# Performance work log

Measured on AMD Instinct MI355X. Metric: run time of the kernel, lower is better.

The kernel has to match this reference:

```python
import jax, jax.numpy as jnp
import numpy as np

WORKSPACE_RADIUS = 1.0
WORKSPACE_HEIGHT = 1.0


def setup_inputs() -> dict:
    key = jax.random.key(0)
    k1, k2 = jax.random.split(key)
    # (B, N, 6): xyz + normals, already padded to common length N
    pointclouds = jax.random.normal(k1, (32, 131072, 6), dtype=jnp.float32)
    # (B, 4, 4): homogeneous task transforms
    task_transform = jax.random.normal(k2, (32, 4, 4), dtype=jnp.float32)
    return {"pointclouds": pointclouds, "task_transform": task_transform}


def reference(pointclouds, task_transform):
    # Split xyz points and normals
    pts = pointclouds[..., :3]          # (B, N, 3)
    nrm = pointclouds[..., 3:]          # (B, N, 3)

    rot = task_transform[:, :3, :3]     # (B, 3, 3)
    trans = task_transform[:, :3, 3]    # (B, 3)

    # points @ rotation + translation (matches torch.matmul(points, rotation))
    p = jnp.einsum('bnd,bde->bne', pts, rot) + trans[:, None, :]

    # padded rows have all-zero normals
    non_padded = jnp.sum(nrm, axis=-1) != 0

    sq_dist = p[..., 0] ** 2 + p[..., 1] ** 2
    in_range = (sq_dist < WORKSPACE_RADIUS ** 2) & (p[..., 2] < WORKSPACE_HEIGHT)
    valid = in_range & non_padded      # (B, N)

    # Filter-and-repad: compact valid points to the front (stable = order
    # preserving, as in the torch boolean-index version), zero the tail.
    order = jnp.argsort(~valid, axis=1, stable=True)                 # (B, N)
    gathered = jnp.take_along_axis(pointclouds, order[..., None], axis=1)
    mask_sorted = jnp.take_along_axis(valid, order, axis=1)
    return gathered * mask_sorted[..., None].astype(pointclouds.dtype)
```

## Files before the change

### kernel.cpp

```cpp
#include <hip/hip_runtime.h>
#include <cstdint>

namespace {

constexpr int kB   = 32;
constexpr int kN   = 131072;
constexpr int kC   = 6;
constexpr int TPB  = 256;
constexpr int ROWS_PER_BLK = 512;
constexpr int BPB  = kN / ROWS_PER_BLK;
constexpr int NBLK = kB * BPB;
constexpr int WAVES = TPB / 64;
constexpr int F4_PER_BLK = ROWS_PER_BLK * kC / 4;

__device__ __forceinline__ int waveSum(int v) {
#pragma unroll
    for (int off = 32; off; off >>= 1) v += __shfl_xor(v, off, 64);
    return v;
}


__global__ __launch_bounds__(TPB) void k_count_stage(const float* __restrict__ pc,
                                                     const float* __restrict__ tt,
                                                     float* __restrict__ staged,
                                                     int* __restrict__ blkCnt) {
    const int blk  = blockIdx.x;
    const int b    = blk >> 8;
    const int tid  = threadIdx.x;
    const int lane = tid & 63;
    const int wv   = tid >> 6;

    const float* T = tt + b * 16;
    const float T0 = T[0], T1 = T[1], T2 = T[2],  T3  = T[3];
    const float T4 = T[4], T5 = T[5], T6 = T[6],  T7  = T[7];
    const float T8 = T[8], T9 = T[9], T10 = T[10], T11 = T[11];

    const float4* f4 = (const float4*)pc + (size_t)blk * F4_PER_BLK;
    const float4 qa = f4[tid];
    const float4 qb = f4[tid + 256];
    const float4 qc = f4[tid + 512];

    __shared__ float4 sb[F4_PER_BLK];
    sb[tid] = qa; sb[tid + 256] = qb; sb[tid + 512] = qc;
    __syncthreads();

    const float2* s2 = (const float2*)sb;
    const float2 r0a = s2[6 * tid],     r0b = s2[6 * tid + 1], r0c = s2[6 * tid + 2];
    const float2 r1a = s2[6 * tid + 3], r1b = s2[6 * tid + 4], r1c = s2[6 * tid + 5];

    const float ns0 = (r0b.y + r0c.x) + r0c.y;
    const float px0 = r0a.x * T0 + r0a.y * T4 + r0b.x * T8  + T3;
    const float py0 = r0a.x * T1 + r0a.y * T5 + r0b.x * T9  + T7;
    const float pz0 = r0a.x * T2 + r0a.y * T6 + r0b.x * T10 + T11;
    const bool v0 = (px0 * px0 + py0 * py0 < 1.0f) && (pz0 < 1.0f) && (ns0 != 0.0f);

    const float ns1 = (r1b.y + r1c.x) + r1c.y;
    const float px1 = r1a.x * T0 + r1a.y * T4 + r1b.x * T8  + T3;
    const float py1 = r1a.x * T1 + r1a.y * T5 + r1b.x * T9  + T7;
    const float pz1 = r1a.x * T2 + r1a.y * T6 + r1b.x * T10 + T11;
    const bool v1 = (px1 * px1 + py1 * py1 < 1.0f) && (pz1 < 1.0f) && (ns1 != 0.0f);

    const uint64_t m0 = __ballot(v0);
    const uint64_t m1 = __ballot(v1);

    __shared__ uint64_t sm[WAVES * 2];
    if (lane == 0) { sm[wv * 2] = m0; sm[wv * 2 + 1] = m1; }
    __syncthreads();

    if (wv == 0) {
        int v = (lane < 8) ? __popcll(sm[lane]) : 0;
        v = waveSum(v);
        if (lane == 0) blkCnt[blk] = v;
    }

    int wb = 0;
#pragma unroll
    for (int w = 0; w < WAVES - 1; ++w)
        if (w < wv) wb += __popcll(sm[w * 2]) + __popcll(sm[w * 2 + 1]);
    const uint64_t low = (1ull << lane) - 1ull;
    const int beforeE = __popcll(m0 & low) + __popcll(m1 & low);
    const int rk0 = wb + beforeE;
    const int rk1 = rk0 + (v0 ? 1 : 0);

    float2* st = (float2*)(staged + (size_t)blk * (ROWS_PER_BLK * kC));
    if (v0) { float2* o = st + rk0 * 3; o[0] = r0a; o[1] = r0b; o[2] = r0c; }
    if (v1) { float2* o = st + rk1 * 3; o[0] = r1a; o[1] = r1b; o[2] = r1c; }
}

__global__ __launch_bounds__(TPB) void k_emit(const float* __restrict__ staged,
                                              const int* __restrict__ blkCnt,
                                              float* __restrict__ out) {
    const int blk  = blockIdx.x;
    const int b    = blk >> 8;
    const int sub  = blk & (BPB - 1);
    const int tid  = threadIdx.x;
    const int lane = tid & 63;
    const int wv   = tid >> 6;

    __shared__ int sRed[2 * WAVES];

    const int c = blkCnt[b * BPB + tid];
    const int pw = waveSum((tid < sub) ? c : 0);
    const int tw = waveSum(c);
    if (lane == 0) { sRed[wv] = pw; sRed[WAVES + wv] = tw; }
    __syncthreads();
    const int blockBase = (sRed[0] + sRed[1]) + (sRed[2] + sRed[3]);
    const int total     = (sRed[4] + sRed[5]) + (sRed[6] + sRed[7]);
    const int myCnt     = blkCnt[blk];

    const size_t batchF = (size_t)b * kN * kC;

    const float2* src = (const float2*)(staged + (size_t)blk * (ROWS_PER_BLK * kC));
    float2* dst = (float2*)(out + batchF + (size_t)blockBase * kC);
    const int nf2 = myCnt * 3;
    for (int i = tid; i < nf2; i += TPB) dst[i] = src[i];

    const int tail = kN - total;
    const int len  = (tail + BPB - 1) >> 8;
    const int r0 = total + sub * len;
    const int r1 = min(r0 + len, kN);
    if (r0 < r1) {
        float* base = out + batchF;
        const int f0 = r0 * 6, f1 = r1 * 6;
        if (tid == 0) {
            const float2 zz = make_float2(0.0f, 0.0f);
            if (f0 & 3) *(float2*)(base + f0) = zz;
            if (f1 & 3) *(float2*)(base + (f1 & ~3)) = zz;
        }
        const int a4 = (f0 + 3) >> 2;
        const int b4 = f1 >> 2;
        float4* o4 = (float4*)base;
        const float4 z4 = make_float4(0.0f, 0.0f, 0.0f, 0.0f);
        for (int i = a4 + tid; i < b4; i += TPB) o4[i] = z4;
    }
}


__global__ __launch_bounds__(TPB) void k_count(const float* __restrict__ pc,
                                               const float* __restrict__ tt,
                                               uint64_t* __restrict__ masks,
                                               int* __restrict__ blkCnt) {
    const int blk  = blockIdx.x;
    const int b    = blk >> 8;
    const int tid  = threadIdx.x;
    const int lane = tid & 63;
    const int wv   = tid >> 6;

    const float* T = tt + b * 16;
    const float T0 = T[0], T1 = T[1], T2 = T[2],  T3  = T[3];
    const float T4 = T[4], T5 = T[5], T6 = T[6],  T7  = T[7];
    const float T8 = T[8], T9 = T[9], T10 = T[10], T11 = T[11];

    const float4* f4 = (const float4*)pc + (size_t)blk * F4_PER_BLK;
    const float4 q0 = f4[3 * tid];
    const float4 q1 = f4[3 * tid + 1];
    const float4 q2 = f4[3 * tid + 2];

    const float ns0 = (q0.w + q1.x) + q1.y;
    const float px0 = q0.x * T0 + q0.y * T4 + q0.z * T8  + T3;
    const float py0 = q0.x * T1 + q0.y * T5 + q0.z * T9  + T7;
    const float pz0 = q0.x * T2 + q0.y * T6 + q0.z * T10 + T11;
    const bool v0 = (px0 * px0 + py0 * py0 < 1.0f) && (pz0 < 1.0f) && (ns0 != 0.0f);

    const float ns1 = (q2.y + q2.z) + q2.w;
    const float px1 = q1.z * T0 + q1.w * T4 + q2.x * T8  + T3;
    const float py1 = q1.z * T1 + q1.w * T5 + q2.x * T9  + T7;
    const float pz1 = q1.z * T2 + q1.w * T6 + q2.x * T10 + T11;
    const bool v1 = (px1 * px1 + py1 * py1 < 1.0f) && (pz1 < 1.0f) && (ns1 != 0.0f);

    const uint64_t m0 = __ballot(v0);
    const uint64_t m1 = __ballot(v1);

    __shared__ uint64_t sm[WAVES * 2];
    if (lane == 0) {
        sm[wv * 2]     = m0;
        sm[wv * 2 + 1] = m1;
        masks[(size_t)blk * 8 + wv * 2]     = m0;
        masks[(size_t)blk * 8 + wv * 2 + 1] = m1;
    }
    __syncthreads();
    if (wv == 0) {
        int v = (lane < 8) ? __popcll(sm[lane]) : 0;
        v = waveSum(v);
        if (lane == 0) blkCnt[blk] = v;
    }
}

__global__ __launch_bounds__(TPB) void k_scatter(const float* __restrict__ pc,
                                                 const uint64_t* __restrict__ masks,
                                                 const int* __restrict__ blkCnt,
                                                 float* __restrict__ out) {
    const int blk  = blockIdx.x;
    const int b    = blk >> 8;
    const int sub  = blk & (BPB - 1);
    const int tid  = threadIdx.x;
    const int lane = tid & 63;
    const int wv   = tid >> 6;

    __shared__ uint64_t sm[8];
    __shared__ int sRed[2 * WAVES];

    if (tid < 8) sm[tid] = masks[(size_t)blk * 8 + tid];

    const int c = blkCnt[b * BPB + tid];
    const int pw = waveSum((tid < sub) ? c : 0);
    const int tw = waveSum(c);
    if (lane == 0) { sRed[wv] = pw; sRed[WAVES + wv] = tw; }
    __syncthreads();
    const int blockBase = (sRed[0] + sRed[1]) + (sRed[2] + sRed[3]);
    const int total     = (sRed[4] + sRed[5]) + (sRed[6] + sRed[7]);

    const uint64_t m0 = sm[wv * 2], m1 = sm[wv * 2 + 1];
    int wb = 0;
#pragma unroll
    for (int w = 0; w < WAVES - 1; ++w)
        if (w < wv) wb += __popcll(sm[w * 2]) + __popcll(sm[w * 2 + 1]);

    const uint64_t low = (1ull << lane) - 1ull;
    const int beforeE = __popcll(m0 & low) + __popcll(m1 & low);
    const bool v0 = (m0 >> lane) & 1ull;
    const bool v1 = (m1 >> lane) & 1ull;

    const size_t batchF = (size_t)b * kN * kC;
    const int rowBlk = sub * ROWS_PER_BLK + wv * 128 + 2 * lane;
    const int vcnt0 = blockBase + wb + beforeE;
    const int vcnt1 = vcnt0 + (v0 ? 1 : 0);

    if (v0) {
        const float2* r = (const float2*)(pc + batchF + (size_t)rowBlk * kC);
        float2* o = (float2*)(out + batchF + (size_t)vcnt0 * kC);
        o[0] = r[0]; o[1] = r[1]; o[2] = r[2];
    }
    if (v1) {
        const float2* r = (const float2*)(pc + batchF + (size_t)(rowBlk + 1) * kC);
        float2* o = (float2*)(out + batchF + (size_t)vcnt1 * kC);
        o[0] = r[0]; o[1] = r[1]; o[2] = r[2];
    }

    const int tail = kN - total;
    const int len  = (tail + BPB - 1) >> 8;
    const int r0 = total + sub * len;
    const int r1 = min(r0 + len, kN);
    if (r0 < r1) {
        float* base = out + batchF;
        const int f0 = r0 * 6, f1 = r1 * 6;
        if (tid == 0) {
            const float2 zz = make_float2(0.0f, 0.0f);
            if (f0 & 3) *(float2*)(base + f0) = zz;
            if (f1 & 3) *(float2*)(base + (f1 & ~3)) = zz;
        }
        const int a4 = (f0 + 3) >> 2;
        const int b4 = f1 >> 2;
        float4* o4 = (float4*)base;
        const float4 z4 = make_float4(0.0f, 0.0f, 0.0f, 0.0f);
        for (int i = a4 + tid; i < b4; i += TPB) o4[i] = z4;
    }
}

}

extern "C" void kernel_launch(void* const* d_in, const int* in_sizes, int n_in,
                              void* d_out, int out_size, void* d_ws, size_t ws_size,
                              hipStream_t stream) {
    const float* pc = (const float*)d_in[0];
    const float* tt = (const float*)d_in[1];
    float* out = (float*)d_out;

    const size_t stagedBytes = (size_t)NBLK * ROWS_PER_BLK * kC * sizeof(float);
    const size_t cntBytes    = (size_t)NBLK * sizeof(int);

    if (ws_size >= stagedBytes + cntBytes) {
        float* staged = (float*)d_ws;
        int* blkCnt   = (int*)((char*)d_ws + stagedBytes);
        k_count_stage<<<NBLK, TPB, 0, stream>>>(pc, tt, staged, blkCnt);
        k_emit<<<NBLK, TPB, 0, stream>>>(staged, blkCnt, out);
    } else {
        uint64_t* masks = (uint64_t*)d_ws;
        int* blkCnt     = (int*)((char*)d_ws + (size_t)NBLK * 8 * sizeof(uint64_t));
        k_count<<<NBLK, TPB, 0, stream>>>(pc, tt, masks, blkCnt);
        k_scatter<<<NBLK, TPB, 0, stream>>>(pc, masks, blkCnt, out);
    }
}
```

Before: 37.49 us.

## Rewrite emit as output-owned gather with binary search over block prefix sums

The emit kernel now assigns each thread two output rows instead of copying each staged block's compacted rows to a variable offset and zero-filling a separate tail range. It builds a full prefix scan of block counts in shared memory, binary-searches for the source block of each output row, gathers from the staged buffer, and writes zeros past the valid count. The goal is fully coalesced, aligned float4 stores with uniform work per block and no separate tail pass. The cost is an 8-step shared-memory search per row and scattered staged reads across block boundaries.

```diff
diff --git a/kernel.cpp b/kernel.cpp
--- a/kernel.cpp
+++ b/kernel.cpp
@@ -12,6 +12,7 @@
 constexpr int NBLK = kB * BPB;
 constexpr int WAVES = TPB / 64;
 constexpr int F4_PER_BLK = ROWS_PER_BLK * kC / 4;
+constexpr int F2_PER_SLOT = ROWS_PER_BLK * kC / 2;
 
 __device__ __forceinline__ int waveSum(int v) {
 #pragma unroll
@@ -97,7 +98,125 @@
     const int lane = tid & 63;
     const int wv   = tid >> 6;
 
+    __shared__ int pre[BPB];
+    __shared__ int wsum[WAVES];
+    __shared__ int s_tot;
+
+    const int c = blkCnt[b * BPB + tid];
+    int v = c;
+#pragma unroll
+    for (int off = 1; off < 64; off <<= 1) {
+        const int u = __shfl_up(v, off, 64);
+        if (lane >= off) v += u;
+    }
+    if (lane == 63) wsum[wv] = v;
+    __syncthreads();
+    int wbase = 0;
+#pragma unroll
+    for (int w = 0; w < WAVES - 1; ++w)
+        if (w < wv) wbase += wsum[w];
+    pre[tid] = wbase + v - c;
+    if (tid == TPB - 1) s_tot = wbase + v;
+    __syncthreads();
+    const int total = s_tot;
+
+    const size_t batchF = (size_t)b * kN * kC;
+    const int r0 = sub * ROWS_PER_BLK + 2 * tid;
+
+    float2 val[6];
+#pragma unroll
+    for (int e = 0; e < 2; ++e) {
+        const int r = r0 + e;
+        float2 x0 = make_float2(0.0f, 0.0f), x1 = x0, x2 = x0;
+        if (r < total) {
+            int lo = 0, hi = BPB - 1;
+#pragma unroll
+            for (int it = 0; it < 8; ++it) {
+                const int mid = (lo + hi + 1) >> 1;
+                if (pre[mid] <= r) lo = mid; else hi = mid - 1;
+            }
+            const int local = r - pre[lo];
+            const float2* s = (const float2*)staged
+                            + (size_t)(b * BPB + lo) * F2_PER_SLOT + (size_t)local * 3;
+            x0 = s[0]; x1 = s[1]; x2 = s[2];
+        }
+        val[3 * e]     = x0;
+        val[3 * e + 1] = x1;
+        val[3 * e + 2] = x2;
+    }
+
+    float4* o4 = (float4*)(out + batchF + (size_t)r0 * kC);
+    o4[0] = make_float4(val[0].x, val[0].y, val[1].x, val[1].y);
+    o4[1] = make_float4(val[2].x, val[2].y, val[3].x, val[3].y);
+    o4[2] = make_float4(val[4].x, val[4].y, val[5].x, val[5].y);
+}
+
+
+__global__ __launch_bounds__(TPB) void k_count(const float* __restrict__ pc,
+                                               const float* __restrict__ tt,
+                                               uint64_t* __restrict__ masks,
+                                               int* __restrict__ blkCnt) {
+    const int blk  = blockIdx.x;
+    const int b    = blk >> 8;
+    const int tid  = threadIdx.x;
+    const int lane = tid & 63;
+    const int wv   = tid >> 6;
+
+    const float* T = tt + b * 16;
+    const float T0 = T[0], T1 = T[1], T2 = T[2],  T3  = T[3];
+    const float T4 = T[4], T5 = T[5], T6 = T[6],  T7  = T[7];
+    const float T8 = T[8], T9 = T[9], T10 = T[10], T11 = T[11];
+
+    const float4* f4 = (const float4*)pc + (size_t)blk * F4_PER_BLK;
+    const float4 q0 = f4[3 * tid];
+    const float4 q1 = f4[3 * tid + 1];
+    const float4 q2 = f4[3 * tid + 2];
+
+    const float ns0 = (q0.w + q1.x) + q1.y;
+    const float px0 = q0.x * T0 + q0.y * T4 + q0.z * T8  + T3;
+    const float py0 = q0.x * T1 + q0.y * T5 + q0.z * T9  + T7;
+    const float pz0 = q0.x * T2 + q0.y * T6 + q0.z * T10 + T11;
+    const bool v0 = (px0 * px0 + py0 * py0 < 1.0f) && (pz0 < 1.0f) && (ns0 != 0.0f);
+
+    const float ns1 = (q2.y + q2.z) + q2.w;
+    const float px1 = q1.z * T0 + q1.w * T4 + q2.x * T8  + T3;
+    const float py1 = q1.z * T1 + q1.w * T5 + q2.x * T9  + T7;
+    const float pz1 = q1.z * T2 + q1.w * T6 + q2.x * T10 + T11;
+    const bool v1 = (px1 * px1 + py1 * py1 < 1.0f) && (pz1 < 1.0f) && (ns1 != 0.0f);
+
+    const uint64_t m0 = __ballot(v0);
+    const uint64_t m1 = __ballot(v1);
+
+    __shared__ uint64_t sm[WAVES * 2];
+    if (lane == 0) {
+        sm[wv * 2]     = m0;
+        sm[wv * 2 + 1] = m1;
+        masks[(size_t)blk * 8 + wv * 2]     = m0;
+        masks[(size_t)blk * 8 + wv * 2 + 1] = m1;
+    }
+    __syncthreads();
+    if (wv == 0) {
+        int v = (lane < 8) ? __popcll(sm[lane]) : 0;
+        v = waveSum(v);
+        if (lane == 0) blkCnt[blk] = v;
+    }
+}
+
+__global__ __launch_bounds__(TPB) void k_scatter(const float* __restrict__ pc,
+                                                 const uint64_t* __restrict__ masks,
+                                                 const int* __restrict__ blkCnt,
+                                                 float* __restrict__ out) {
+    const int blk  = blockIdx.x;
+    const int b    = blk >> 8;
+    const int sub  = blk & (BPB - 1);
+    const int tid  = threadIdx.x;
+    const int lane = tid & 63;
+    const int wv   = tid >> 6;
+
+    __shared__ uint64_t sm[8];
     __shared__ int sRed[2 * WAVES];
+
+    if (tid < 8) sm[tid] = masks[(size_t)blk * 8 + tid];
 
     const int c = blkCnt[b * BPB + tid];
     const int pw = waveSum((tid < sub) ? c : 0);
@@ -106,14 +225,33 @@
     __syncthreads();
     const int blockBase = (sRed[0] + sRed[1]) + (sRed[2] + sRed[3]);
     const int total     = (sRed[4] + sRed[5]) + (sRed[6] + sRed[7]);
-    const int myCnt     = blkCnt[blk];
+
+    const uint64_t m0 = sm[wv * 2], m1 = sm[wv * 2 + 1];
+    int wb = 0;
+#pragma unroll
+    for (int w = 0; w < WAVES - 1; ++w)
+        if (w < wv) wb += __popcll(sm[w * 2]) + __popcll(sm[w * 2 + 1]);
+
+    const uint64_t low = (1ull << lane) - 1ull;
+    const int beforeE = __popcll(m0 & low) + __popcll(m1 & low);
+    const bool v0 = (m0 >> lane) & 1ull;
+    const bool v1 = (m1 >> lane) & 1ull;
 
     const size_t batchF = (size_t)b * kN * kC;
-
-    const float2* src = (const float2*)(staged + (size_t)blk * (ROWS_PER_BLK * kC));
-    float2* dst = (float2*)(out + batchF + (size_t)blockBase * kC);
-    const int nf2 = myCnt * 3;
-    for (int i = tid; i < nf2; i += TPB) dst[i] = src[i];
+    const int rowBlk = sub * ROWS_PER_BLK + wv * 128 + 2 * lane;
+    const int vcnt0 = blockBase + wb + beforeE;
+    const int vcnt1 = vcnt0 + (v0 ? 1 : 0);
+
+    if (v0) {
+        const float2* r = (const float2*)(pc + batchF + (size_t)rowBlk * kC);
+        float2* o = (float2*)(out + batchF + (size_t)vcnt0 * kC);
+        o[0] = r[0]; o[1] = r[1]; o[2] = r[2];
+    }
+    if (v1) {
+        const float2* r = (const float2*)(pc + batchF + (size_t)(rowBlk + 1) * kC);
+        float2* o = (float2*)(out + batchF + (size_t)vcnt1 * kC);
+        o[0] = r[0]; o[1] = r[1]; o[2] = r[2];
+    }
 
     const int tail = kN - total;
     const int len  = (tail + BPB - 1) >> 8;
@@ -135,128 +273,6 @@
     }
 }
 
-
-__global__ __launch_bounds__(TPB) void k_count(const float* __restrict__ pc,
-                                               const float* __restrict__ tt,
-                                               uint64_t* __restrict__ masks,
-                                               int* __restrict__ blkCnt) {
-    const int blk  = blockIdx.x;
-    const int b    = blk >> 8;
-    const int tid  = threadIdx.x;
-    const int lane = tid & 63;
-    const int wv   = tid >> 6;
-
-    const float* T = tt + b * 16;
-    const float T0 = T[0], T1 = T[1], T2 = T[2],  T3  = T[3];
-    const float T4 = T[4], T5 = T[5], T6 = T[6],  T7  = T[7];
-    const float T8 = T[8], T9 = T[9], T10 = T[10], T11 = T[11];
-
-    const float4* f4 = (const float4*)pc + (size_t)blk * F4_PER_BLK;
-    const float4 q0 = f4[3 * tid];
-    const float4 q1 = f4[3 * tid + 1];
-    const float4 q2 = f4[3 * tid + 2];
-
-    const float ns0 = (q0.w + q1.x) + q1.y;
-    const float px0 = q0.x * T0 + q0.y * T4 + q0.z * T8  + T3;
-    const float py0 = q0.x * T1 + q0.y * T5 + q0.z * T9  + T7;
-    const float pz0 = q0.x * T2 + q0.y * T6 + q0.z * T10 + T11;
-    const bool v0 = (px0 * px0 + py0 * py0 < 1.0f) && (pz0 < 1.0f) && (ns0 != 0.0f);
-
-    const float ns1 = (q2.y + q2.z) + q2.w;
-    const float px1 = q1.z * T0 + q1.w * T4 + q2.x * T8  + T3;
-    const float py1 = q1.z * T1 + q1.w * T5 + q2.x * T9  + T7;
-    const float pz1 = q1.z * T2 + q1.w * T6 + q2.x * T10 + T11;
-    const bool v1 = (px1 * px1 + py1 * py1 < 1.0f) && (pz1 < 1.0f) && (ns1 != 0.0f);
-
-    const uint64_t m0 = __ballot(v0);
-    const uint64_t m1 = __ballot(v1);
-
-    __shared__ uint64_t sm[WAVES * 2];
-    if (lane == 0) {
-        sm[wv * 2]     = m0;
-        sm[wv * 2 + 1] = m1;
-        masks[(size_t)blk * 8 + wv * 2]     = m0;
-        masks[(size_t)blk * 8 + wv * 2 + 1] = m1;
-    }
-    __syncthreads();
-    if (wv == 0) {
-        int v = (lane < 8) ? __popcll(sm[lane]) : 0;
-        v = waveSum(v);
-        if (lane == 0) blkCnt[blk] = v;
-    }
-}
-
-__global__ __launch_bounds__(TPB) void k_scatter(const float* __restrict__ pc,
-                                                 const uint64_t* __restrict__ masks,
-                                                 const int* __restrict__ blkCnt,
-                                                 float* __restrict__ out) {
-    const int blk  = blockIdx.x;
-    const int b    = blk >> 8;
-    const int sub  = blk & (BPB - 1);
-    const int tid  = threadIdx.x;
-    const int lane = tid & 63;
-    const int wv   = tid >> 6;
-
-    __shared__ uint64_t sm[8];
-    __shared__ int sRed[2 * WAVES];
-
-    if (tid < 8) sm[tid] = masks[(size_t)blk * 8 + tid];
-
-    const int c = blkCnt[b * BPB + tid];
-    const int pw = waveSum((tid < sub) ? c : 0);
-    const int tw = waveSum(c);
-    if (lane == 0) { sRed[wv] = pw; sRed[WAVES + wv] = tw; }
-    __syncthreads();
-    const int blockBase = (sRed[0] + sRed[1]) + (sRed[2] + sRed[3]);
-    const int total     = (sRed[4] + sRed[5]) + (sRed[6] + sRed[7]);
-
-    const uint64_t m0 = sm[wv * 2], m1 = sm[wv * 2 + 1];
-    int wb = 0;
-#pragma unroll
-    for (int w = 0; w < WAVES - 1; ++w)
-        if (w < wv) wb += __popcll(sm[w * 2]) + __popcll(sm[w * 2 + 1]);
-
-    const uint64_t low = (1ull << lane) - 1ull;
-    const int beforeE = __popcll(m0 & low) + __popcll(m1 & low);
-    const bool v0 = (m0 >> lane) & 1ull;
-    const bool v1 = (m1 >> lane) & 1ull;
-
-    const size_t batchF = (size_t)b * kN * kC;
-    const int rowBlk = sub * ROWS_PER_BLK + wv * 128 + 2 * lane;
-    const int vcnt0 = blockBase + wb + beforeE;
-    const int vcnt1 = vcnt0 + (v0 ? 1 : 0);
-
-    if (v0) {
-        const float2* r = (const float2*)(pc + batchF + (size_t)rowBlk * kC);
-        float2* o = (float2*)(out + batchF + (size_t)vcnt0 * kC);
-        o[0] = r[0]; o[1] = r[1]; o[2] = r[2];
-    }
-    if (v1) {
-        const float2* r = (const float2*)(pc + batchF + (size_t)(rowBlk + 1) * kC);
-        float2* o = (float2*)(out + batchF + (size_t)vcnt1 * kC);
-        o[0] = r[0]; o[1] = r[1]; o[2] = r[2];
-    }
-
-    const int tail = kN - total;
-    const int len  = (tail + BPB - 1) >> 8;
-    const int r0 = total + sub * len;
-    const int r1 = min(r0 + len, kN);
-    if (r0 < r1) {
-        float* base = out + batchF;
-        const int f0 = r0 * 6, f1 = r1 * 6;
-        if (tid == 0) {
-            const float2 zz = make_float2(0.0f, 0.0f);
-            if (f0 & 3) *(float2*)(base + f0) = zz;
-            if (f1 & 3) *(float2*)(base + (f1 & ~3)) = zz;
-        }
-        const int a4 = (f0 + 3) >> 2;
-        const int b4 = f1 >> 2;
-        float4* o4 = (float4*)base;
-        const float4 z4 = make_float4(0.0f, 0.0f, 0.0f, 0.0f);
-        for (int i = a4 + tid; i < b4; i += TPB) o4[i] = z4;
-    }
-}
-
 }
 
 extern "C" void kernel_launch(void* const* d_in, const int* in_sizes, int n_in,
```

Measured after the change: 47.82 us. 1.28x slower.
